# Kernel optimization log

Hardware: AMD Instinct MI355X
Metric: run time of the kernel (lower is better)

Reference implementation:

```python
import jax, jax.numpy as jnp
import numpy as np

# Geometry constants (match module defaults)
PCR = (0.0, -40.0, -3.0, 70.4, 40.0, 1.0)
VX, VY, VZ = 0.2, 0.2, 4.0
GX, GY, GZ = 352, 400, 1  # canvas_x/y/z per module's round() formulas
B = 2
N = 400000
C0, C1 = 64, 128
IN_CH = 10  # 4 raw + 3 cluster + 3 voxel-center
CANVAS = B * GZ * GY * GX
X_OFF = VX / 2 + PCR[0]
Y_OFF = VY / 2 + PCR[1]
Z_OFF = VZ / 2 + PCR[2]
BN_EPS = 1e-3


def setup_inputs() -> dict:
    key = jax.random.key(0)
    ks = jax.random.split(key, 8)
    x = jax.random.uniform(ks[0], (N,), minval=PCR[0], maxval=PCR[3] - 1e-3)
    y = jax.random.uniform(ks[1], (N,), minval=PCR[1], maxval=PCR[4] - 1e-3)
    z = jax.random.uniform(ks[2], (N,), minval=PCR[2], maxval=PCR[5] - 1e-3)
    inten = jax.random.uniform(ks[3], (N,))
    bidx = (jnp.arange(N) * B // N).astype(jnp.float32)  # sorted batch column
    points = jnp.stack([bidx, x, y, z, inten], axis=1).astype(jnp.float32)
    W0 = jax.random.normal(ks[4], (IN_CH, C0), dtype=jnp.float32) / np.sqrt(IN_CH)
    W1 = jax.random.normal(ks[5], (2 * C0, C1), dtype=jnp.float32) / np.sqrt(2 * C0)
    return {
        "points": points,
        "W0": W0, "g0": jnp.ones((C0,), jnp.float32), "b0": jnp.zeros((C0,), jnp.float32),
        "W1": W1, "g1": jnp.ones((C1,), jnp.float32), "b1": jnp.zeros((C1,), jnp.float32),
    }


def _vfe_layer(x, W, gamma, beta):
    # Linear(bias=False) -> BatchNorm1d(train-mode, eps=1e-3) -> ReLU
    h = x @ W
    mu = jnp.mean(h, axis=0)
    var = jnp.var(h, axis=0)
    h = (h - mu) * jax.lax.rsqrt(var + BN_EPS) * gamma + beta
    return jax.nn.relu(h)


def _forward(points, W0, g0, b0, W1, g1, b1):
    b = points[:, 0].astype(jnp.int32)
    xyz = points[:, 1:4]
    feats4 = points[:, 1:5]
    # dynamic voxelization: per-point voxel coordinates
    cx = jnp.clip(jnp.floor((points[:, 1] - PCR[0]) / VX), 0, GX - 1).astype(jnp.int32)
    cy = jnp.clip(jnp.floor((points[:, 2] - PCR[1]) / VY), 0, GY - 1).astype(jnp.int32)
    cz = jnp.clip(jnp.floor((points[:, 3] - PCR[2]) / VZ), 0, GZ - 1).astype(jnp.int32)
    vidx = ((b * GZ + cz) * GY + cy) * GX + cx  # flat canvas index per point

    count = jax.ops.segment_sum(jnp.ones((points.shape[0],), points.dtype), vidx,
                                num_segments=CANVAS)
    occupied = count > 0

    # cluster_scatter: mean of xyz per voxel, gathered back to points
    vox_mean = jax.ops.segment_sum(xyz, vidx, num_segments=CANVAS)
    vox_mean = vox_mean / jnp.maximum(count, 1.0)[:, None]
    f_cluster = xyz - vox_mean[vidx]

    # offset to voxel center
    vcen = jnp.stack([
        cx.astype(points.dtype) * VX + X_OFF,
        cy.astype(points.dtype) * VY + Y_OFF,
        cz.astype(points.dtype) * VZ + Z_OFF,
    ], axis=1)
    f_center = xyz - vcen

    feats = jnp.concatenate([feats4, f_cluster, f_center], axis=1)  # [N, 10]

    # VFE layer 0 -> scatter-max -> gather-back -> concat
    pf0 = _vfe_layer(feats, W0, g0, b0)  # [N, 64]
    vmax0 = jax.ops.segment_max(pf0, vidx, num_segments=CANVAS)
    vmax0 = jnp.where(occupied[:, None], vmax0, 0.0)
    feats1 = jnp.concatenate([pf0, vmax0[vidx]], axis=1)  # [N, 128]

    # VFE layer 1 -> final scatter-max over voxels
    pf1 = _vfe_layer(feats1, W1, g1, b1)  # [N, 128]
    vmax1 = jax.ops.segment_max(pf1, vidx, num_segments=CANVAS)
    voxel_feats = jnp.where(occupied[:, None], vmax1, 0.0)  # [CANVAS, 128] dense canvas
    return voxel_feats


def reference(points, W0, g0, b0, W1, g1, b1):
    return _forward(points, W0, g0, b0, W1, g1, b1)
```

## Files before the change

kernel.cpp:

```cpp
#include <hip/hip_runtime.h>
#include <hip/hip_fp16.h>
#include <stdint.h>

#define NPTS 400000
#define NVOX 281600
#define TPB  256
#define NBLK ((NPTS + TPB - 1) / TPB)
#define SCANB (NVOX / 256)
#define STRETCH 64
#define FBLK (NPTS / STRETCH)
#define SBLK2 1024

typedef _Float16 h8  __attribute__((ext_vector_type(8)));
typedef _Float16 h4v __attribute__((ext_vector_type(4)));
typedef float    f4  __attribute__((ext_vector_type(4)));

__device__ __forceinline__ int bin3(const float* __restrict__ pt,
                                    int& bx, int& by, int& bz) {
  float x = pt[1], y = pt[2], z = pt[3];
  bx = (int)fminf(fmaxf(floorf(x * 5.0f), 0.f), 351.f);
  by = (int)fminf(fmaxf(floorf((y + 40.f) * 5.0f), 0.f), 399.f);
  bz = (int)fminf(fmaxf(floorf((z + 3.f) * 0.25f), 0.f), 0.f);
  return (((int)pt[0] + bz) * 400 + by) * 352 + bx;
}

__device__ __forceinline__ int mkfeat(const float* __restrict__ pt,
    const float* __restrict__ vcnt, const float* __restrict__ vsx,
    const float* __restrict__ vsy, const float* __restrict__ vsz,
    float* f) {
  int bx, by, bz;
  int v = bin3(pt, bx, by, bz);
  float x = pt[1], y = pt[2], z = pt[3];
  float n = fmaxf(vcnt[v], 1.f);
  f[0] = x;  f[1] = y;  f[2] = z;  f[3] = pt[4];
  f[4] = x - vsx[v] / n;
  f[5] = y - vsy[v] / n;
  f[6] = z - vsz[v] / n;
  f[7] = x - (0.2f * (float)bx + 0.1f);
  f[8] = y - (0.2f * (float)by - 39.9f);
  f[9] = z - (4.0f * (float)bz - 1.0f);
  return v;
}

__global__ __launch_bounds__(256) void voxsum(const float* __restrict__ pts,
    float* __restrict__ vcnt, float* __restrict__ vsx,
    float* __restrict__ vsy, float* __restrict__ vsz) {
  int p = blockIdx.x * TPB + threadIdx.x;
  if (p >= NPTS) return;
  const float* pt = pts + (size_t)p * 5;
  int bx, by, bz;
  int v = bin3(pt, bx, by, bz);
  atomicAdd(&vcnt[v], 1.f);
  atomicAdd(&vsx[v], pt[1]);
  atomicAdd(&vsy[v], pt[2]);
  atomicAdd(&vsz[v], pt[3]);
}

__global__ __launch_bounds__(256) void bn0stats(const float* __restrict__ pts,
    const float* __restrict__ vcnt, const float* __restrict__ vsx,
    const float* __restrict__ vsy, const float* __restrict__ vsz,
    const float* __restrict__ W0,
    double* __restrict__ gs, double* __restrict__ gq) {
  __shared__ float bs[4][64], bq[4][64];
  int t = threadIdx.x, wv = t >> 6, ln = t & 63;
  int p = blockIdx.x * TPB + t;
  bool ok = p < NPTS;
  const float* pt = pts + (size_t)(ok ? p : 0) * 5;
  float f[10];
  mkfeat(pt, vcnt, vsx, vsy, vsz, f);
  for (int c = 0; c < 64; ++c) {
    float h = f[0] * W0[c];
    #pragma unroll
    for (int i = 1; i < 10; ++i) h = fmaf(f[i], W0[i * 64 + c], h);
    h = ok ? h : 0.f;
    float q = h * h;
    #pragma unroll
    for (int m = 1; m < 64; m <<= 1) {
      h += __shfl_xor(h, m, 64);
      q += __shfl_xor(q, m, 64);
    }
    if (ln == 0) { bs[wv][c] = h; bq[wv][c] = q; }
  }
  __syncthreads();
  if (t < 64) {
    atomicAdd(&gs[t], (double)bs[0][t] + bs[1][t] + bs[2][t] + bs[3][t]);
    atomicAdd(&gq[t], (double)bq[0][t] + bq[1][t] + bq[2][t] + bq[3][t]);
  }
}

__global__ void bnfold(const double* __restrict__ gs, const double* __restrict__ gq,
                       const float* __restrict__ gam, const float* __restrict__ bet,
                       float* __restrict__ sc, float* __restrict__ sh, int C) {
  int c = threadIdx.x;
  if (c >= C) return;
  double mu  = gs[c] / (double)NPTS;
  double var = gq[c] / (double)NPTS - mu * mu;
  double s = (double)gam[c] / sqrt(var + 1e-3);
  sc[c] = (float)s;
  sh[c] = (float)((double)bet[c] - mu * s);
}

__global__ __launch_bounds__(256) void scan1(const float* __restrict__ vcnt,
    unsigned int* __restrict__ voxloc, unsigned int* __restrict__ bsum) {
  __shared__ unsigned int s[256];
  int t = threadIdx.x;
  int i = blockIdx.x * 256 + t;
  unsigned int val = (unsigned int)vcnt[i];
  s[t] = val;
  __syncthreads();
  for (int off = 1; off < 256; off <<= 1) {
    unsigned int add = (t >= off) ? s[t - off] : 0u;
    __syncthreads();
    s[t] += add;
    __syncthreads();
  }
  voxloc[i] = s[t] - val;
  if (t == 255) bsum[blockIdx.x] = s[t];
}

__global__ void scan2(const unsigned int* __restrict__ bsum,
                      unsigned int* __restrict__ bexc) {
  if (threadIdx.x != 0) return;
  unsigned int run = 0;
  for (int b = 0; b < SCANB; ++b) { bexc[b] = run; run += bsum[b]; }
}

__global__ __launch_bounds__(256) void prep(const float* __restrict__ vcnt,
    const unsigned int* __restrict__ voxloc, const unsigned int* __restrict__ bexc,
    float* __restrict__ vmax, float* __restrict__ outp) {
  int v = blockIdx.x * 256 + threadIdx.x;
  int n = (int)vcnt[v];
  f4 z = {0, 0, 0, 0};
  if (n == 0) {
    f4* o = (f4*)(outp + (size_t)v * 128);
    #pragma unroll
    for (int i = 0; i < 32; ++i) o[i] = z;
    return;
  }
  unsigned int vstart = voxloc[v] + bexc[v >> 8];
  bool interior = ((vstart & (STRETCH - 1)) + (unsigned)n) <= STRETCH;
  if (!interior) {
    f4* o = (f4*)(outp + (size_t)v * 128);
    #pragma unroll
    for (int i = 0; i < 32; ++i) o[i] = z;
    f4* m = (f4*)(vmax + (size_t)v * 64);
    #pragma unroll
    for (int i = 0; i < 16; ++i) m[i] = z;
  }
}

__global__ __launch_bounds__(256) void scatter(const float* __restrict__ pts,
    const unsigned int* __restrict__ voxloc, const unsigned int* __restrict__ bexc,
    unsigned int* __restrict__ cursor, unsigned int* __restrict__ plist,
    unsigned int* __restrict__ vsort) {
  int p = blockIdx.x * TPB + threadIdx.x;
  if (p >= NPTS) return;
  int bx, by, bz;
  int v = bin3(pts + (size_t)p * 5, bx, by, bz);
  unsigned int pos = voxloc[v] + bexc[v >> 8] + atomicAdd(&cursor[v], 1u);
  plist[pos] = (unsigned int)p;
  vsort[pos] = (unsigned int)v;
}

__global__ __launch_bounds__(256) void vmax0_stretch(const float* __restrict__ pts,
    const float* __restrict__ vcnt, const float* __restrict__ vsx,
    const float* __restrict__ vsy, const float* __restrict__ vsz,
    const unsigned int* __restrict__ voxloc, const unsigned int* __restrict__ bexc,
    const unsigned int* __restrict__ plist,
    const float* __restrict__ W0, const float* __restrict__ sc0,
    const float* __restrict__ sh0, float* __restrict__ vmax) {
  __shared__ float sf[STRETCH][12];
  __shared__ int   svid[STRETCH];
  __shared__ float pf[STRETCH][64];
  int t = threadIdx.x;
  unsigned int sbeg = blockIdx.x * STRETCH;

  if (t < STRETCH) {
    unsigned int pidx = plist[sbeg + t];
    svid[t] = mkfeat(pts + (size_t)pidx * 5, vcnt, vsx, vsy, vsz, &sf[t][0]);
  }
  __syncthreads();
  for (int idx = t; idx < STRETCH * 64; idx += TPB) {
    int pt_ = idx >> 6, k = idx & 63;
    float h = sf[pt_][0] * W0[k];
    #pragma unroll
    for (int i = 1; i < 10; ++i) h = fmaf(sf[pt_][i], W0[i * 64 + k], h);
    pf[pt_][k] = fmaxf(fmaf(h, sc0[k], sh0[k]), 0.f);
  }
  __syncthreads();

  if (t < 64) {
    int curv = -1; float curm = 0.f;
    for (int i = 0; i < STRETCH; ++i) {
      int v = svid[i];
      if (v != curv) {
        if (curv >= 0) {
          unsigned int vstart = voxloc[curv] + bexc[curv >> 8];
          unsigned int n = (unsigned int)vcnt[curv];
          if (vstart >= sbeg && vstart + n <= sbeg + STRETCH)
            vmax[(size_t)curv * 64 + t] = curm;
          else
            atomicMax((unsigned int*)&vmax[(size_t)curv * 64 + t],
                      __float_as_uint(curm));
        }
        curv = v;
        curm = pf[i][t];
      } else {
        curm = fmaxf(curm, pf[i][t]);
      }
    }
    if (curv >= 0) {
      unsigned int vstart = voxloc[curv] + bexc[curv >> 8];
      unsigned int n = (unsigned int)vcnt[curv];
      if (vstart >= sbeg && vstart + n <= sbeg + STRETCH)
        vmax[(size_t)curv * 64 + t] = curm;
      else
        atomicMax((unsigned int*)&vmax[(size_t)curv * 64 + t],
                  __float_as_uint(curm));
    }
  }
}

__global__ __launch_bounds__(256) void wconv(const float* __restrict__ W1,
                                             _Float16* __restrict__ Wf) {
  int idx = blockIdx.x * 256 + threadIdx.x;
  if (idx >= 32 * 64 * 8) return;
  int j = idx & 7, l = (idx >> 3) & 63, f = idx >> 9;
  int ks = f & 3, ntile = f >> 2;
  int k = ks * 32 + ((j >> 2) * 16) + 4 * (l >> 4) + (j & 3);
  int n = ntile * 16 + (l & 15);
  Wf[idx] = (_Float16)W1[k * 128 + n];
}

__device__ __forceinline__ h8 lda(const _Float16* __restrict__ r, int k0) {
  h4v lo = *(const h4v*)(r + k0);
  h4v hi = *(const h4v*)(r + k0 + 16);
  h8 a;
  a[0] = lo[0]; a[1] = lo[1]; a[2] = lo[2]; a[3] = lo[3];
  a[4] = hi[0]; a[5] = hi[1]; a[6] = hi[2]; a[7] = hi[3];
  return a;
}

__device__ __forceinline__ void emit_tile(f4 C, int ptb, int ch,
    _Float16* __restrict__ h1o, float& sf_, float& qf_) {
  float v0 = C[0], v1 = C[1], v2 = C[2], v3 = C[3];
  h1o[(size_t)(ptb + 0) * 128 + ch] = (_Float16)v0;
  h1o[(size_t)(ptb + 1) * 128 + ch] = (_Float16)v1;
  h1o[(size_t)(ptb + 2) * 128 + ch] = (_Float16)v2;
  h1o[(size_t)(ptb + 3) * 128 + ch] = (_Float16)v3;
  sf_ += (v0 + v1) + (v2 + v3);
  qf_ = fmaf(v0, v0, fmaf(v1, v1, fmaf(v2, v2, fmaf(v3, v3, qf_))));
}

__global__ __launch_bounds__(256) void gemm1m(const float* __restrict__ pts,
    const float* __restrict__ vcnt, const float* __restrict__ vsx,
    const float* __restrict__ vsy, const float* __restrict__ vsz,
    const unsigned int* __restrict__ plist,
    const float* __restrict__ W0, const float* __restrict__ sc0,
    const float* __restrict__ sh0, const float* __restrict__ vmax,
    const _Float16* __restrict__ Wf,
    double* __restrict__ gs, double* __restrict__ gq,
    _Float16* __restrict__ h1out) {
  __shared__ float sf[STRETCH][12];
  __shared__ int   svid[STRETCH];
  __shared__ __align__(16) _Float16 fh[64][140];

  int t = threadIdx.x;
  int w = t >> 6, l = t & 63;
  int lm = l & 15, lg = l >> 4;

  const h8* wfv = (const h8*)Wf;
  h8 B00 = wfv[((w * 2 + 0) * 4 + 0) * 64 + l];
  h8 B01 = wfv[((w * 2 + 0) * 4 + 1) * 64 + l];
  h8 B02 = wfv[((w * 2 + 0) * 4 + 2) * 64 + l];
  h8 B03 = wfv[((w * 2 + 0) * 4 + 3) * 64 + l];
  h8 B10 = wfv[((w * 2 + 1) * 4 + 0) * 64 + l];
  h8 B11 = wfv[((w * 2 + 1) * 4 + 1) * 64 + l];
  h8 B12 = wfv[((w * 2 + 1) * 4 + 2) * 64 + l];
  h8 B13 = wfv[((w * 2 + 1) * 4 + 3) * 64 + l];

  double sd0 = 0, sd1 = 0, qd0 = 0, qd1 = 0;

  for (int tile = blockIdx.x; tile < FBLK; tile += gridDim.x) {
    unsigned int sbeg = tile * STRETCH;
    if (t < STRETCH) {
      unsigned int pidx = plist[sbeg + t];
      svid[t] = mkfeat(pts + (size_t)pidx * 5, vcnt, vsx, vsy, vsz, &sf[t][0]);
    }
    __syncthreads();
    for (int idx = t; idx < STRETCH * 64; idx += TPB) {
      int p_ = idx >> 6, k = idx & 63;
      float h = sf[p_][0] * W0[k];
      #pragma unroll
      for (int i = 1; i < 10; ++i) h = fmaf(sf[p_][i], W0[i * 64 + k], h);
      fh[p_][k] = (_Float16)fmaxf(fmaf(h, sc0[k], sh0[k]), 0.f);
    }
    for (int idx = t; idx < STRETCH * 64; idx += TPB) {
      int p_ = idx >> 6, k = idx & 63;
      fh[p_][64 + k] = (_Float16)vmax[(size_t)svid[p_] * 64 + k];
    }
    __syncthreads();

    f4 C00 = {0,0,0,0}, C01 = {0,0,0,0}, C10 = {0,0,0,0}, C11 = {0,0,0,0};
    f4 C20 = {0,0,0,0}, C21 = {0,0,0,0}, C30 = {0,0,0,0}, C31 = {0,0,0,0};

    #define DO_MT(mt, CA, CB) {                                              \
      const _Float16* r = &fh[(mt) * 16 + lm][0];                            \
      h8 A0 = lda(r, 0 * 32 + 4 * lg);                                       \
      h8 A1 = lda(r, 1 * 32 + 4 * lg);                                       \
      h8 A2 = lda(r, 2 * 32 + 4 * lg);                                       \
      h8 A3 = lda(r, 3 * 32 + 4 * lg);                                       \
      CA = __builtin_amdgcn_mfma_f32_16x16x32_f16(A0, B00, CA, 0, 0, 0);     \
      CA = __builtin_amdgcn_mfma_f32_16x16x32_f16(A1, B01, CA, 0, 0, 0);     \
      CA = __builtin_amdgcn_mfma_f32_16x16x32_f16(A2, B02, CA, 0, 0, 0);     \
      CA = __builtin_amdgcn_mfma_f32_16x16x32_f16(A3, B03, CA, 0, 0, 0);     \
      CB = __builtin_amdgcn_mfma_f32_16x16x32_f16(A0, B10, CB, 0, 0, 0);     \
      CB = __builtin_amdgcn_mfma_f32_16x16x32_f16(A1, B11, CB, 0, 0, 0);     \
      CB = __builtin_amdgcn_mfma_f32_16x16x32_f16(A2, B12, CB, 0, 0, 0);     \
      CB = __builtin_amdgcn_mfma_f32_16x16x32_f16(A3, B13, CB, 0, 0, 0); }
    DO_MT(0, C00, C01)
    DO_MT(1, C10, C11)
    DO_MT(2, C20, C21)
    DO_MT(3, C30, C31)
    #undef DO_MT

    float s0f = 0, q0f = 0, s1f = 0, q1f = 0;
    int ch0 = w * 32 + lm, ch1 = w * 32 + 16 + lm;
    emit_tile(C00, sbeg + 0 * 16 + lg * 4, ch0, h1out, s0f, q0f);
    emit_tile(C01, sbeg + 0 * 16 + lg * 4, ch1, h1out, s1f, q1f);
    emit_tile(C10, sbeg + 1 * 16 + lg * 4, ch0, h1out, s0f, q0f);
    emit_tile(C11, sbeg + 1 * 16 + lg * 4, ch1, h1out, s1f, q1f);
    emit_tile(C20, sbeg + 2 * 16 + lg * 4, ch0, h1out, s0f, q0f);
    emit_tile(C21, sbeg + 2 * 16 + lg * 4, ch1, h1out, s1f, q1f);
    emit_tile(C30, sbeg + 3 * 16 + lg * 4, ch0, h1out, s0f, q0f);
    emit_tile(C31, sbeg + 3 * 16 + lg * 4, ch1, h1out, s1f, q1f);
    sd0 += (double)s0f; qd0 += (double)q0f;
    sd1 += (double)s1f; qd1 += (double)q1f;
    __syncthreads();
  }

  sd0 += __shfl_xor(sd0, 16, 64); sd0 += __shfl_xor(sd0, 32, 64);
  qd0 += __shfl_xor(qd0, 16, 64); qd0 += __shfl_xor(qd0, 32, 64);
  sd1 += __shfl_xor(sd1, 16, 64); sd1 += __shfl_xor(sd1, 32, 64);
  qd1 += __shfl_xor(qd1, 16, 64); qd1 += __shfl_xor(qd1, 32, 64);
  if (lg == 0) {
    atomicAdd(&gs[w * 32 + lm], sd0);
    atomicAdd(&gq[w * 32 + lm], qd0);
    atomicAdd(&gs[w * 32 + 16 + lm], sd1);
    atomicAdd(&gq[w * 32 + 16 + lm], qd1);
  }
}

__global__ __launch_bounds__(256) void final_cheap(
    const unsigned int* __restrict__ vsort,
    const unsigned int* __restrict__ voxloc, const unsigned int* __restrict__ bexc,
    const float* __restrict__ vcnt, const _Float16* __restrict__ h1,
    const float* __restrict__ sc1, const float* __restrict__ sh1,
    float* __restrict__ outp) {
  int t = threadIdx.x, w = t >> 6, l = t & 63;
  int s = blockIdx.x * 4 + w;
  if (s >= FBLK) return;
  unsigned int sbeg = (unsigned int)s * STRETCH;
  float2 sv = *(const float2*)(sc1 + 2 * l);
  float2 bv = *(const float2*)(sh1 + 2 * l);

  int curv = -1; float m0 = 0.f, m1 = 0.f;
  #define FLUSH()                                                            \
    { unsigned int vstart = voxloc[curv] + bexc[curv >> 8];                  \
      unsigned int n = (unsigned int)vcnt[curv];                             \
      if (vstart >= sbeg && vstart + n <= sbeg + STRETCH) {                  \
        *(float2*)(outp + (size_t)curv * 128 + 2 * l) = make_float2(m0, m1); \
      } else {                                                               \
        atomicMax((unsigned int*)&outp[(size_t)curv * 128 + 2 * l],          \
                  __float_as_uint(m0));                                      \
        atomicMax((unsigned int*)&outp[(size_t)curv * 128 + 2 * l + 1],      \
                  __float_as_uint(m1));                                      \
      } }
  for (int i = 0; i < STRETCH; ++i) {
    int v = (int)vsort[sbeg + i];
    __half2 hv = *(const __half2*)(h1 + (size_t)(sbeg + i) * 128 + 2 * l);
    float2 hf = __half22float2(hv);
    float v0 = fmaxf(fmaf(hf.x, sv.x, bv.x), 0.f);
    float v1 = fmaxf(fmaf(hf.y, sv.y, bv.y), 0.f);
    if (v != curv) {
      if (curv >= 0) FLUSH()
      curv = v; m0 = v0; m1 = v1;
    } else {
      m0 = fmaxf(m0, v0);
      m1 = fmaxf(m1, v1);
    }
  }
  if (curv >= 0) FLUSH()
  #undef FLUSH
}

#define TILE_STAGE(sbeg_)                                                    \
  if (t < STRETCH) {                                                         \
    unsigned int pidx = plist[(sbeg_) + t];                                  \
    svid[t] = mkfeat(pts + (size_t)pidx * 5, vcnt, vsx, vsy, vsz, &sf[t][0]);\
  }                                                                          \
  __syncthreads();                                                           \
  for (int idx = t; idx < STRETCH * 64; idx += TPB) {                        \
    int pt_ = idx >> 6, k = idx & 63;                                        \
    float h = sf[pt_][0] * W0[k];                                            \
    _Pragma("unroll")                                                        \
    for (int i = 1; i < 10; ++i) h = fmaf(sf[pt_][i], W0[i * 64 + k], h);    \
    sfeat[pt_][k] = fmaxf(fmaf(h, sc0[k], sh0[k]), 0.f);                     \
  }                                                                          \
  for (int idx = t; idx < STRETCH * 64; idx += TPB) {                        \
    int pt_ = idx >> 6, k = idx & 63;                                        \
    sfeat[pt_][64 + k] = vmax[(size_t)svid[pt_] * 64 + k];                   \
  }                                                                          \
  __syncthreads();

#define TILE_GEMM()                                                          \
  const float* r0 = sfeat[pg * 8 + 0];                                       \
  const float* r1 = sfeat[pg * 8 + 1];                                       \
  const float* r2 = sfeat[pg * 8 + 2];                                       \
  const float* r3 = sfeat[pg * 8 + 3];                                       \
  const float* r4 = sfeat[pg * 8 + 4];                                       \
  const float* r5 = sfeat[pg * 8 + 5];                                       \
  const float* r6 = sfeat[pg * 8 + 6];                                       \
  const float* r7 = sfeat[pg * 8 + 7];                                       \
  float4 A0 = {0,0,0,0}, A1 = {0,0,0,0}, A2 = {0,0,0,0}, A3 = {0,0,0,0};     \
  float4 A4 = {0,0,0,0}, A5 = {0,0,0,0}, A6 = {0,0,0,0}, A7 = {0,0,0,0};     \
  _Pragma("unroll 8")                                                        \
  for (int k = 0; k < 128; ++k) {                                            \
    float4 w = *reinterpret_cast<const float4*>(W1 + (size_t)k * 128 + cb*4);\
    float p0 = r0[k], p1_ = r1[k], p2 = r2[k], p3 = r3[k];                   \
    float p4 = r4[k], p5 = r5[k], p6 = r6[k], p7 = r7[k];                    \
    A0.x = fmaf(p0, w.x, A0.x); A0.y = fmaf(p0, w.y, A0.y);                  \
    A0.z = fmaf(p0, w.z, A0.z); A0.w = fmaf(p0, w.w, A0.w);                  \
    A1.x = fmaf(p1_, w.x, A1.x); A1.y = fmaf(p1_, w.y, A1.y);                \
    A1.z = fmaf(p1_, w.z, A1.z); A1.w = fmaf(p1_, w.w, A1.w);                \
    A2.x = fmaf(p2, w.x, A2.x); A2.y = fmaf(p2, w.y, A2.y);                  \
    A2.z = fmaf(p2, w.z, A2.z); A2.w = fmaf(p2, w.w, A2.w);                  \
    A3.x = fmaf(p3, w.x, A3.x); A3.y = fmaf(p3, w.y, A3.y);                  \
    A3.z = fmaf(p3, w.z, A3.z); A3.w = fmaf(p3, w.w, A3.w);                  \
    A4.x = fmaf(p4, w.x, A4.x); A4.y = fmaf(p4, w.y, A4.y);                  \
    A4.z = fmaf(p4, w.z, A4.z); A4.w = fmaf(p4, w.w, A4.w);                  \
    A5.x = fmaf(p5, w.x, A5.x); A5.y = fmaf(p5, w.y, A5.y);                  \
    A5.z = fmaf(p5, w.z, A5.z); A5.w = fmaf(p5, w.w, A5.w);                  \
    A6.x = fmaf(p6, w.x, A6.x); A6.y = fmaf(p6, w.y, A6.y);                  \
    A6.z = fmaf(p6, w.z, A6.z); A6.w = fmaf(p6, w.w, A6.w);                  \
    A7.x = fmaf(p7, w.x, A7.x); A7.y = fmaf(p7, w.y, A7.y);                  \
    A7.z = fmaf(p7, w.z, A7.z); A7.w = fmaf(p7, w.w, A7.w);                  \
  }

__global__ __launch_bounds__(256) void gemm1s_f32(const float* __restrict__ pts,
    const float* __restrict__ vcnt, const float* __restrict__ vsx,
    const float* __restrict__ vsy, const float* __restrict__ vsz,
    const unsigned int* __restrict__ plist,
    const float* __restrict__ W0, const float* __restrict__ sc0,
    const float* __restrict__ sh0, const float* __restrict__ vmax,
    const float* __restrict__ W1,
    double* __restrict__ gs, double* __restrict__ gq) {
  union SM {
    struct { float sf[STRETCH][12]; int svid[STRETCH]; float sfeat[STRETCH][128]; } a;
    struct { double lsum[8 * 128]; double lsq[8 * 128]; } b;
  };
  __shared__ SM sm;
  auto& sf = sm.a.sf;
  auto& svid = sm.a.svid;
  auto& sfeat = sm.a.sfeat;

  int t = threadIdx.x;
  int pg = t >> 5, cb = t & 31;
  double sd0 = 0, sd1 = 0, sd2 = 0, sd3 = 0;
  double qd0 = 0, qd1 = 0, qd2 = 0, qd3 = 0;

  for (int tile = blockIdx.x; tile < FBLK; tile += gridDim.x) {
    unsigned int sbeg = tile * STRETCH;
    TILE_STAGE(sbeg)
    TILE_GEMM()
    sd0 += (double)A0.x + (double)A1.x + (double)A2.x + (double)A3.x
         + (double)A4.x + (double)A5.x + (double)A6.x + (double)A7.x;
    sd1 += (double)A0.y + (double)A1.y + (double)A2.y + (double)A3.y
         + (double)A4.y + (double)A5.y + (double)A6.y + (double)A7.y;
    sd2 += (double)A0.z + (double)A1.z + (double)A2.z + (double)A3.z
         + (double)A4.z + (double)A5.z + (double)A6.z + (double)A7.z;
    sd3 += (double)A0.w + (double)A1.w + (double)A2.w + (double)A3.w
         + (double)A4.w + (double)A5.w + (double)A6.w + (double)A7.w;
    qd0 += (double)A0.x*A0.x + (double)A1.x*A1.x + (double)A2.x*A2.x + (double)A3.x*A3.x
         + (double)A4.x*A4.x + (double)A5.x*A5.x + (double)A6.x*A6.x + (double)A7.x*A7.x;
    qd1 += (double)A0.y*A0.y + (double)A1.y*A1.y + (double)A2.y*A2.y + (double)A3.y*A3.y
         + (double)A4.y*A4.y + (double)A5.y*A5.y + (double)A6.y*A6.y + (double)A7.y*A7.y;
    qd2 += (double)A0.z*A0.z + (double)A1.z*A1.z + (double)A2.z*A2.z + (double)A3.z*A3.z
         + (double)A4.z*A4.z + (double)A5.z*A5.z + (double)A6.z*A6.z + (double)A7.z*A7.z;
    qd3 += (double)A0.w*A0.w + (double)A1.w*A1.w + (double)A2.w*A2.w + (double)A3.w*A3.w
         + (double)A4.w*A4.w + (double)A5.w*A5.w + (double)A6.w*A6.w + (double)A7.w*A7.w;
    __syncthreads();
  }

  int c = cb * 4;
  sm.b.lsum[pg * 128 + c + 0] = sd0;  sm.b.lsq[pg * 128 + c + 0] = qd0;
  sm.b.lsum[pg * 128 + c + 1] = sd1;  sm.b.lsq[pg * 128 + c + 1] = qd1;
  sm.b.lsum[pg * 128 + c + 2] = sd2;  sm.b.lsq[pg * 128 + c + 2] = qd2;
  sm.b.lsum[pg * 128 + c + 3] = sd3;  sm.b.lsq[pg * 128 + c + 3] = qd3;
  __syncthreads();
  if (t < 128) {
    double S = 0, Q = 0;
    #pragma unroll
    for (int j = 0; j < 8; ++j) { S += sm.b.lsum[j * 128 + t]; Q += sm.b.lsq[j * 128 + t]; }
    atomicAdd(&gs[t], S);
    atomicAdd(&gq[t], Q);
  }
}

__global__ __launch_bounds__(256) void final2(const float* __restrict__ pts,
    const float* __restrict__ vcnt, const float* __restrict__ vsx,
    const float* __restrict__ vsy, const float* __restrict__ vsz,
    const unsigned int* __restrict__ voxloc, const unsigned int* __restrict__ bexc,
    const unsigned int* __restrict__ plist,
    const float* __restrict__ W0, const float* __restrict__ sc0,
    const float* __restrict__ sh0, const float* __restrict__ vmax,
    const float* __restrict__ W1, const float* __restrict__ sc1,
    const float* __restrict__ sh1, float* __restrict__ outp) {
  __shared__ float sf[STRETCH][12];
  __shared__ int   svid[STRETCH];
  __shared__ float sfeat[STRETCH][128];

  int t = threadIdx.x;
  int pg = t >> 5, cb = t & 31;
  unsigned int sbeg = blockIdx.x * STRETCH;

  TILE_STAGE(sbeg)
  TILE_GEMM()
  __syncthreads();

  int c = cb * 4;
  float4 s1v = *reinterpret_cast<const float4*>(sc1 + c);
  float4 h1v = *reinterpret_cast<const float4*>(sh1 + c);
  #define BNST(Aj, j)                                                        \
    { float4 P;                                                              \
      P.x = fmaxf(fmaf(Aj.x, s1v.x, h1v.x), 0.f);                            \
      P.y = fmaxf(fmaf(Aj.y, s1v.y, h1v.y), 0.f);                            \
      P.z = fmaxf(fmaf(Aj.z, s1v.z, h1v.z), 0.f);                            \
      P.w = fmaxf(fmaf(Aj.w, s1v.w, h1v.w), 0.f);                            \
      *reinterpret_cast<float4*>(&sfeat[pg * 8 + j][c]) = P; }
  BNST(A0, 0) BNST(A1, 1) BNST(A2, 2) BNST(A3, 3)
  BNST(A4, 4) BNST(A5, 5) BNST(A6, 6) BNST(A7, 7)
  #undef BNST
  __syncthreads();

  if (t < 128) {
    int curv = -1; float curm = 0.f;
    for (int i = 0; i < STRETCH; ++i) {
      int v = svid[i];
      if (v != curv) {
        if (curv >= 0) {
          unsigned int vstart = voxloc[curv] + bexc[curv >> 8];
          unsigned int n = (unsigned int)vcnt[curv];
          if (vstart >= sbeg && vstart + n <= sbeg + STRETCH)
            outp[(size_t)curv * 128 + t] = curm;
          else
            atomicMax((unsigned int*)&outp[(size_t)curv * 128 + t],
                      __float_as_uint(curm));
        }
        curv = v;
        curm = sfeat[i][t];
      } else {
        curm = fmaxf(curm, sfeat[i][t]);
      }
    }
    if (curv >= 0) {
      unsigned int vstart = voxloc[curv] + bexc[curv >> 8];
      unsigned int n = (unsigned int)vcnt[curv];
      if (vstart >= sbeg && vstart + n <= sbeg + STRETCH)
        outp[(size_t)curv * 128 + t] = curm;
      else
        atomicMax((unsigned int*)&outp[(size_t)curv * 128 + t],
                  __float_as_uint(curm));
    }
  }
}

extern "C" void kernel_launch(void* const* d_in, const int* in_sizes, int n_in,
                              void* d_out, int out_size, void* d_ws, size_t ws_size,
                              hipStream_t stream) {
  const float* pts = (const float*)d_in[0];
  const float* W0  = (const float*)d_in[1];
  const float* g0  = (const float*)d_in[2];
  const float* b0  = (const float*)d_in[3];
  const float* W1  = (const float*)d_in[4];
  const float* g1  = (const float*)d_in[5];
  const float* b1  = (const float*)d_in[6];

  char* base = (char*)d_ws;
  double* stats = (double*)base;
  float*  fold  = (float*)(base + 3072);
  float*  vcnt  = (float*)(base + 4608);
  float*  vsx   = vcnt + NVOX;
  float*  vsy   = vsx + NVOX;
  float*  vsz   = vsy + NVOX;
  float*  vmax  = vsz + NVOX;
  unsigned int* voxloc = (unsigned int*)(vmax + (size_t)NVOX * 64);
  unsigned int* cursor = voxloc + NVOX;
  unsigned int* plist  = cursor + NVOX;
  unsigned int* vsort  = plist + NPTS;
  unsigned int* bsum   = vsort + NPTS;
  unsigned int* bexc   = bsum + SCANB;
  _Float16* Wf = (_Float16*)(bexc + SCANB);
  _Float16* h1 = Wf + 32 * 64 * 8;
  size_t need_fast = (size_t)((char*)h1 - base) + (size_t)NPTS * 128 * sizeof(_Float16);
  bool fast = ws_size >= need_fast;

  double* s0 = stats,       *q0 = stats + 64;
  double* s1 = stats + 128, *q1 = stats + 256;
  float* sc0 = fold,       *sh0 = fold + 64;
  float* sc1 = fold + 128, *sh1 = fold + 256;

  hipMemsetAsync(stats, 0, 3072, stream);
  hipMemsetAsync(vcnt, 0, (size_t)4 * NVOX * sizeof(float), stream);
  hipMemsetAsync(cursor, 0, (size_t)NVOX * sizeof(unsigned int), stream);

  voxsum<<<NBLK, TPB, 0, stream>>>(pts, vcnt, vsx, vsy, vsz);
  scan1<<<SCANB, 256, 0, stream>>>(vcnt, voxloc, bsum);
  scan2<<<1, 64, 0, stream>>>(bsum, bexc);
  prep<<<SCANB, 256, 0, stream>>>(vcnt, voxloc, bexc, vmax, (float*)d_out);
  scatter<<<NBLK, TPB, 0, stream>>>(pts, voxloc, bexc, cursor, plist, vsort);
  bn0stats<<<NBLK, TPB, 0, stream>>>(pts, vcnt, vsx, vsy, vsz, W0, s0, q0);
  bnfold<<<1, 64, 0, stream>>>(s0, q0, g0, b0, sc0, sh0, 64);
  vmax0_stretch<<<FBLK, TPB, 0, stream>>>(pts, vcnt, vsx, vsy, vsz, voxloc, bexc,
                                          plist, W0, sc0, sh0, vmax);
  if (fast) {
    wconv<<<64, 256, 0, stream>>>(W1, Wf);
    gemm1m<<<SBLK2, TPB, 0, stream>>>(pts, vcnt, vsx, vsy, vsz, plist,
                                      W0, sc0, sh0, vmax, Wf, s1, q1, h1);
    bnfold<<<1, 128, 0, stream>>>(s1, q1, g1, b1, sc1, sh1, 128);
    final_cheap<<<(FBLK + 3) / 4, 256, 0, stream>>>(vsort, voxloc, bexc, vcnt,
                                                    h1, sc1, sh1, (float*)d_out);
  } else {
    gemm1s_f32<<<SBLK2, TPB, 0, stream>>>(pts, vcnt, vsx, vsy, vsz, plist,
                                          W0, sc0, sh0, vmax, W1, s1, q1);
    bnfold<<<1, 128, 0, stream>>>(s1, q1, g1, b1, sc1, sh1, 128);
    final2<<<FBLK, TPB, 0, stream>>>(pts, vcnt, vsx, vsy, vsz, voxloc, bexc,
                                     plist, W0, sc0, sh0, vmax, W1, sc1, sh1,
                                     (float*)d_out);
  }
}
```

Baseline: 420.1 us.

## Cache layer-0 point features in fp16 and load MFMA operands directly from global

```diff
diff --git a/kernel.cpp b/kernel.cpp
--- a/kernel.cpp
+++ b/kernel.cpp
@@ -168,7 +168,8 @@
     const unsigned int* __restrict__ voxloc, const unsigned int* __restrict__ bexc,
     const unsigned int* __restrict__ plist,
     const float* __restrict__ W0, const float* __restrict__ sc0,
-    const float* __restrict__ sh0, float* __restrict__ vmax) {
+    const float* __restrict__ sh0, float* __restrict__ vmax,
+    _Float16* __restrict__ pf0h) {
   __shared__ float sf[STRETCH][12];
   __shared__ int   svid[STRETCH];
   __shared__ float pf[STRETCH][64];
@@ -185,7 +186,9 @@
     float h = sf[pt_][0] * W0[k];
     #pragma unroll
     for (int i = 1; i < 10; ++i) h = fmaf(sf[pt_][i], W0[i * 64 + k], h);
-    pf[pt_][k] = fmaxf(fmaf(h, sc0[k], sh0[k]), 0.f);
+    float val = fmaxf(fmaf(h, sc0[k], sh0[k]), 0.f);
+    pf[pt_][k] = val;
+    pf0h[(size_t)(sbeg + pt_) * 64 + k] = (_Float16)val;
   }
   __syncthreads();
 
@@ -232,12 +235,18 @@
   Wf[idx] = (_Float16)W1[k * 128 + n];
 }
 
-__device__ __forceinline__ h8 lda(const _Float16* __restrict__ r, int k0) {
-  h4v lo = *(const h4v*)(r + k0);
-  h4v hi = *(const h4v*)(r + k0 + 16);
+__device__ __forceinline__ h8 mk8(h4v lo, h4v hi) {
   h8 a;
   a[0] = lo[0]; a[1] = lo[1]; a[2] = lo[2]; a[3] = lo[3];
   a[4] = hi[0]; a[5] = hi[1]; a[6] = hi[2]; a[7] = hi[3];
+  return a;
+}
+__device__ __forceinline__ h8 mk8f(f4 lo, f4 hi) {
+  h8 a;
+  a[0] = (_Float16)lo[0]; a[1] = (_Float16)lo[1];
+  a[2] = (_Float16)lo[2]; a[3] = (_Float16)lo[3];
+  a[4] = (_Float16)hi[0]; a[5] = (_Float16)hi[1];
+  a[6] = (_Float16)hi[2]; a[7] = (_Float16)hi[3];
   return a;
 }
 
@@ -252,19 +261,12 @@
   qf_ = fmaf(v0, v0, fmaf(v1, v1, fmaf(v2, v2, fmaf(v3, v3, qf_))));
 }
 
-__global__ __launch_bounds__(256) void gemm1m(const float* __restrict__ pts,
-    const float* __restrict__ vcnt, const float* __restrict__ vsx,
-    const float* __restrict__ vsy, const float* __restrict__ vsz,
-    const unsigned int* __restrict__ plist,
-    const float* __restrict__ W0, const float* __restrict__ sc0,
-    const float* __restrict__ sh0, const float* __restrict__ vmax,
+__global__ __launch_bounds__(256) void gemm1m(
+    const unsigned int* __restrict__ vsort,
+    const _Float16* __restrict__ pf0h, const float* __restrict__ vmax,
     const _Float16* __restrict__ Wf,
     double* __restrict__ gs, double* __restrict__ gq,
     _Float16* __restrict__ h1out) {
-  __shared__ float sf[STRETCH][12];
-  __shared__ int   svid[STRETCH];
-  __shared__ __align__(16) _Float16 fh[64][140];
-
   int t = threadIdx.x;
   int w = t >> 6, l = t & 63;
   int lm = l & 15, lg = l >> 4;
@@ -283,33 +285,20 @@
 
   for (int tile = blockIdx.x; tile < FBLK; tile += gridDim.x) {
     unsigned int sbeg = tile * STRETCH;
-    if (t < STRETCH) {
-      unsigned int pidx = plist[sbeg + t];
-      svid[t] = mkfeat(pts + (size_t)pidx * 5, vcnt, vsx, vsy, vsz, &sf[t][0]);
-    }
-    __syncthreads();
-    for (int idx = t; idx < STRETCH * 64; idx += TPB) {
-      int p_ = idx >> 6, k = idx & 63;
-      float h = sf[p_][0] * W0[k];
-      #pragma unroll
-      for (int i = 1; i < 10; ++i) h = fmaf(sf[p_][i], W0[i * 64 + k], h);
-      fh[p_][k] = (_Float16)fmaxf(fmaf(h, sc0[k], sh0[k]), 0.f);
-    }
-    for (int idx = t; idx < STRETCH * 64; idx += TPB) {
-      int p_ = idx >> 6, k = idx & 63;
-      fh[p_][64 + k] = (_Float16)vmax[(size_t)svid[p_] * 64 + k];
-    }
-    __syncthreads();
 
     f4 C00 = {0,0,0,0}, C01 = {0,0,0,0}, C10 = {0,0,0,0}, C11 = {0,0,0,0};
     f4 C20 = {0,0,0,0}, C21 = {0,0,0,0}, C30 = {0,0,0,0}, C31 = {0,0,0,0};
 
     #define DO_MT(mt, CA, CB) {                                              \
-      const _Float16* r = &fh[(mt) * 16 + lm][0];                            \
-      h8 A0 = lda(r, 0 * 32 + 4 * lg);                                       \
-      h8 A1 = lda(r, 1 * 32 + 4 * lg);                                       \
-      h8 A2 = lda(r, 2 * 32 + 4 * lg);                                       \
-      h8 A3 = lda(r, 3 * 32 + 4 * lg);                                       \
+      unsigned int slot = sbeg + (mt) * 16 + lm;                             \
+      const _Float16* pr = pf0h + (size_t)slot * 64;                         \
+      h8 A0 = mk8(*(const h4v*)(pr + 4 * lg),                                \
+                  *(const h4v*)(pr + 16 + 4 * lg));                          \
+      h8 A1 = mk8(*(const h4v*)(pr + 32 + 4 * lg),                           \
+                  *(const h4v*)(pr + 48 + 4 * lg));                          \
+      const float* vr = vmax + (size_t)vsort[slot] * 64;                     \
+      h8 A2 = mk8f(*(const f4*)(vr + 4 * lg), *(const f4*)(vr + 16 + 4*lg)); \
+      h8 A3 = mk8f(*(const f4*)(vr + 32 + 4*lg), *(const f4*)(vr + 48+4*lg));\
       CA = __builtin_amdgcn_mfma_f32_16x16x32_f16(A0, B00, CA, 0, 0, 0);     \
       CA = __builtin_amdgcn_mfma_f32_16x16x32_f16(A1, B01, CA, 0, 0, 0);     \
       CA = __builtin_amdgcn_mfma_f32_16x16x32_f16(A2, B02, CA, 0, 0, 0);     \
@@ -336,7 +325,6 @@
     emit_tile(C31, sbeg + 3 * 16 + lg * 4, ch1, h1out, s1f, q1f);
     sd0 += (double)s0f; qd0 += (double)q0f;
     sd1 += (double)s1f; qd1 += (double)q1f;
-    __syncthreads();
   }
 
   sd0 += __shfl_xor(sd0, 16, 64); sd0 += __shfl_xor(sd0, 32, 64);
@@ -593,15 +581,17 @@
   float*  vsx   = vcnt + NVOX;
   float*  vsy   = vsx + NVOX;
   float*  vsz   = vsy + NVOX;
-  float*  vmax  = vsz + NVOX;
-  unsigned int* voxloc = (unsigned int*)(vmax + (size_t)NVOX * 64);
-  unsigned int* cursor = voxloc + NVOX;
-  unsigned int* plist  = cursor + NVOX;
+  unsigned int* cursor = (unsigned int*)(vsz + NVOX);
+  size_t zbytes = 4608 + (size_t)5 * NVOX * 4;
+  unsigned int* voxloc = cursor + NVOX;
+  unsigned int* plist  = voxloc + NVOX;
   unsigned int* vsort  = plist + NPTS;
   unsigned int* bsum   = vsort + NPTS;
   unsigned int* bexc   = bsum + SCANB;
-  _Float16* Wf = (_Float16*)(bexc + SCANB);
-  _Float16* h1 = Wf + 32 * 64 * 8;
+  float* vmax = (float*)(bexc + SCANB);
+  _Float16* Wf = (_Float16*)(vmax + (size_t)NVOX * 64);
+  _Float16* pf0h = Wf + 32 * 64 * 8;
+  _Float16* h1 = pf0h + (size_t)NPTS * 64;
   size_t need_fast = (size_t)((char*)h1 - base) + (size_t)NPTS * 128 * sizeof(_Float16);
   bool fast = ws_size >= need_fast;
 
@@ -610,9 +600,7 @@
   float* sc0 = fold,       *sh0 = fold + 64;
   float* sc1 = fold + 128, *sh1 = fold + 256;
 
-  hipMemsetAsync(stats, 0, 3072, stream);
-  hipMemsetAsync(vcnt, 0, (size_t)4 * NVOX * sizeof(float), stream);
-  hipMemsetAsync(cursor, 0, (size_t)NVOX * sizeof(unsigned int), stream);
+  hipMemsetAsync(base, 0, zbytes, stream);
 
   voxsum<<<NBLK, TPB, 0, stream>>>(pts, vcnt, vsx, vsy, vsz);
   scan1<<<SCANB, 256, 0, stream>>>(vcnt, voxloc, bsum);
@@ -622,11 +610,10 @@
   bn0stats<<<NBLK, TPB, 0, stream>>>(pts, vcnt, vsx, vsy, vsz, W0, s0, q0);
   bnfold<<<1, 64, 0, stream>>>(s0, q0, g0, b0, sc0, sh0, 64);
   vmax0_stretch<<<FBLK, TPB, 0, stream>>>(pts, vcnt, vsx, vsy, vsz, voxloc, bexc,
-                                          plist, W0, sc0, sh0, vmax);
+                                          plist, W0, sc0, sh0, vmax, pf0h);
   if (fast) {
     wconv<<<64, 256, 0, stream>>>(W1, Wf);
-    gemm1m<<<SBLK2, TPB, 0, stream>>>(pts, vcnt, vsx, vsy, vsz, plist,
-                                      W0, sc0, sh0, vmax, Wf, s1, q1, h1);
+    gemm1m<<<SBLK2, TPB, 0, stream>>>(vsort, pf0h, vmax, Wf, s1, q1, h1);
     bnfold<<<1, 128, 0, stream>>>(s1, q1, g1, b1, sc1, sh1, 128);
     final_cheap<<<(FBLK + 3) / 4, 256, 0, stream>>>(vsort, voxloc, bexc, vcnt,
                                                     h1, sc1, sh1, (float*)d_out);
```

New measurement: 464.7 us. +10.6%, slower.

## Compute layer-0 BN stats from feature Gram matrix instead of per-channel GEMV

Applied to the files above, without the earlier changes.

```diff
diff --git a/kernel.cpp b/kernel.cpp
--- a/kernel.cpp
+++ b/kernel.cpp
@@ -10,6 +10,7 @@
 #define STRETCH 64
 #define FBLK (NPTS / STRETCH)
 #define SBLK2 1024
+#define GRAMB 64
 
 typedef _Float16 h8  __attribute__((ext_vector_type(8)));
 typedef _Float16 h4v __attribute__((ext_vector_type(4)));
@@ -56,36 +57,89 @@
   atomicAdd(&vsz[v], pt[3]);
 }
 
-__global__ __launch_bounds__(256) void bn0stats(const float* __restrict__ pts,
+__global__ __launch_bounds__(256) void bn0gram(const float* __restrict__ pts,
     const float* __restrict__ vcnt, const float* __restrict__ vsx,
     const float* __restrict__ vsy, const float* __restrict__ vsz,
-    const float* __restrict__ W0,
-    double* __restrict__ gs, double* __restrict__ gq) {
-  __shared__ float bs[4][64], bq[4][64];
+    double* __restrict__ gpart) {
+  __shared__ float sred[4][65];
   int t = threadIdx.x, wv = t >> 6, ln = t & 63;
-  int p = blockIdx.x * TPB + t;
-  bool ok = p < NPTS;
-  const float* pt = pts + (size_t)(ok ? p : 0) * 5;
-  float f[10];
-  mkfeat(pt, vcnt, vsx, vsy, vsz, f);
-  for (int c = 0; c < 64; ++c) {
-    float h = f[0] * W0[c];
-    #pragma unroll
-    for (int i = 1; i < 10; ++i) h = fmaf(f[i], W0[i * 64 + c], h);
-    h = ok ? h : 0.f;
-    float q = h * h;
-    #pragma unroll
-    for (int m = 1; m < 64; m <<= 1) {
-      h += __shfl_xor(h, m, 64);
-      q += __shfl_xor(q, m, 64);
-    }
-    if (ln == 0) { bs[wv][c] = h; bq[wv][c] = q; }
-  }
-  __syncthreads();
-  if (t < 64) {
-    atomicAdd(&gs[t], (double)bs[0][t] + bs[1][t] + bs[2][t] + bs[3][t]);
-    atomicAdd(&gq[t], (double)bq[0][t] + bq[1][t] + bq[2][t] + bq[3][t]);
-  }
+  float s[10], G[55];
+  #pragma unroll
+  for (int i = 0; i < 10; ++i) s[i] = 0.f;
+  #pragma unroll
+  for (int k = 0; k < 55; ++k) G[k] = 0.f;
+
+  for (int p = blockIdx.x * 256 + t; p < NPTS; p += gridDim.x * 256) {
+    float f[10];
+    mkfeat(pts + (size_t)p * 5, vcnt, vsx, vsy, vsz, f);
+    #pragma unroll
+    for (int i = 0; i < 10; ++i) s[i] += f[i];
+    int k = 0;
+    #pragma unroll
+    for (int i = 0; i < 10; ++i) {
+      #pragma unroll
+      for (int j = i; j < 10; ++j) { G[k] = fmaf(f[i], f[j], G[k]); ++k; }
+    }
+  }
+  #pragma unroll
+  for (int i = 0; i < 10; ++i) {
+    #pragma unroll
+    for (int m = 1; m < 64; m <<= 1) s[i] += __shfl_xor(s[i], m, 64);
+  }
+  #pragma unroll
+  for (int k = 0; k < 55; ++k) {
+    #pragma unroll
+    for (int m = 1; m < 64; m <<= 1) G[k] += __shfl_xor(G[k], m, 64);
+  }
+  if (ln == 0) {
+    #pragma unroll
+    for (int i = 0; i < 10; ++i) sred[wv][i] = s[i];
+    #pragma unroll
+    for (int k = 0; k < 55; ++k) sred[wv][10 + k] = G[k];
+  }
+  __syncthreads();
+  if (t < 65) {
+    gpart[(size_t)blockIdx.x * 65 + t] =
+        (double)sred[0][t] + sred[1][t] + sred[2][t] + sred[3][t];
+  }
+}
+
+__global__ void bnfold0g(const double* __restrict__ gpart,
+                         const float* __restrict__ W0,
+                         const float* __restrict__ g0, const float* __restrict__ b0,
+                         float* __restrict__ sc, float* __restrict__ sh) {
+  __shared__ double acc[65];
+  int t = threadIdx.x;
+  if (t < 65) {
+    double a = 0;
+    for (int b = 0; b < GRAMB; ++b) a += gpart[(size_t)b * 65 + t];
+    acc[t] = a;
+  }
+  __syncthreads();
+  if (t >= 64) return;
+  double w[10];
+  #pragma unroll
+  for (int i = 0; i < 10; ++i) w[i] = (double)W0[i * 64 + t];
+  double mu = 0;
+  #pragma unroll
+  for (int i = 0; i < 10; ++i) mu += acc[i] * w[i];
+  mu /= (double)NPTS;
+  double e2 = 0;
+  int k = 0;
+  #pragma unroll
+  for (int i = 0; i < 10; ++i) {
+    #pragma unroll
+    for (int j = i; j < 10; ++j) {
+      double term = acc[10 + k] * w[i] * w[j];
+      e2 += (i == j) ? term : 2.0 * term;
+      ++k;
+    }
+  }
+  e2 /= (double)NPTS;
+  double var = e2 - mu * mu;
+  double sd = (double)g0[t] / sqrt(var + 1e-3);
+  sc[t] = (float)sd;
+  sh[t] = (float)((double)b0[t] - mu * sd);
 }
 
 __global__ void bnfold(const double* __restrict__ gs, const double* __restrict__ gq,
@@ -593,34 +647,33 @@
   float*  vsx   = vcnt + NVOX;
   float*  vsy   = vsx + NVOX;
   float*  vsz   = vsy + NVOX;
-  float*  vmax  = vsz + NVOX;
-  unsigned int* voxloc = (unsigned int*)(vmax + (size_t)NVOX * 64);
-  unsigned int* cursor = voxloc + NVOX;
-  unsigned int* plist  = cursor + NVOX;
+  unsigned int* cursor = (unsigned int*)(vsz + NVOX);
+  size_t zbytes = 4608 + (size_t)5 * NVOX * 4;
+  unsigned int* voxloc = cursor + NVOX;
+  unsigned int* plist  = voxloc + NVOX;
   unsigned int* vsort  = plist + NPTS;
   unsigned int* bsum   = vsort + NPTS;
   unsigned int* bexc   = bsum + SCANB;
-  _Float16* Wf = (_Float16*)(bexc + SCANB);
+  double* gpart = (double*)(bexc + SCANB);
+  float* vmax = (float*)(gpart + GRAMB * 65);
+  _Float16* Wf = (_Float16*)(vmax + (size_t)NVOX * 64);
   _Float16* h1 = Wf + 32 * 64 * 8;
   size_t need_fast = (size_t)((char*)h1 - base) + (size_t)NPTS * 128 * sizeof(_Float16);
   bool fast = ws_size >= need_fast;
 
-  double* s0 = stats,       *q0 = stats + 64;
   double* s1 = stats + 128, *q1 = stats + 256;
   float* sc0 = fold,       *sh0 = fold + 64;
   float* sc1 = fold + 128, *sh1 = fold + 256;
 
-  hipMemsetAsync(stats, 0, 3072, stream);
-  hipMemsetAsync(vcnt, 0, (size_t)4 * NVOX * sizeof(float), stream);
-  hipMemsetAsync(cursor, 0, (size_t)NVOX * sizeof(unsigned int), stream);
+  hipMemsetAsync(base, 0, zbytes, stream);
 
   voxsum<<<NBLK, TPB, 0, stream>>>(pts, vcnt, vsx, vsy, vsz);
   scan1<<<SCANB, 256, 0, stream>>>(vcnt, voxloc, bsum);
   scan2<<<1, 64, 0, stream>>>(bsum, bexc);
   prep<<<SCANB, 256, 0, stream>>>(vcnt, voxloc, bexc, vmax, (float*)d_out);
   scatter<<<NBLK, TPB, 0, stream>>>(pts, voxloc, bexc, cursor, plist, vsort);
-  bn0stats<<<NBLK, TPB, 0, stream>>>(pts, vcnt, vsx, vsy, vsz, W0, s0, q0);
-  bnfold<<<1, 64, 0, stream>>>(s0, q0, g0, b0, sc0, sh0, 64);
+  bn0gram<<<GRAMB, 256, 0, stream>>>(pts, vcnt, vsx, vsy, vsz, gpart);
+  bnfold0g<<<1, 128, 0, stream>>>(gpart, W0, g0, b0, sc0, sh0);
   vmax0_stretch<<<FBLK, TPB, 0, stream>>>(pts, vcnt, vsx, vsy, vsz, voxloc, bexc,
                                           plist, W0, sc0, sh0, vmax);
   if (fast) {
```

Result: faster. 386.8 us (-7.9%).
